# Optimization experiments

Hardware: AMD Instinct MI355X
Metric: run time of the kernel (lower is better)

## Reference

```python
import jax, jax.numpy as jnp
import numpy as np

T, B, C, N, H = 4, 8, 256, 2048, 16
D = C // H          # head dim = 16
SCALE = 0.25        # fixed scale in SCA_AV
EPS = 1e-5          # BatchNorm eps


def _conv_bn(h_in, w, gamma, beta):
    """1x1 Conv1d (bias=False) + BatchNorm1d in training mode.
    h_in: [T,B,C,N]; w: [C_out,C_in]; BN stats over (T,B,N) per channel."""
    h = jnp.einsum('oc,tbcn->tbon', w, h_in)
    mean = h.mean(axis=(0, 1, 3), keepdims=True)
    var = ((h - mean) ** 2).mean(axis=(0, 1, 3), keepdims=True)
    return gamma[None, None, :, None] * (h - mean) * jax.lax.rsqrt(var + EPS) + beta[None, None, :, None]


def _spike(h, vth):
    # MyNode called once after reset: mem = 0/tau + h; spike = (mem >= vth)
    return (h >= vth).astype(h.dtype)


def _heads(z):
    # [T,B,C,N] -> [T,B,H,N,D] (channel index c = h*D + d, matching torch reshape)
    return z.reshape(T, B, H, D, N).transpose(0, 1, 2, 4, 3)


def setup_inputs() -> dict:
    key = jax.random.key(0)
    ks = jax.random.split(key, 16)
    s = 1.0 / np.sqrt(C)
    inp = {
        'x': jax.random.normal(ks[0], (T, B, C, N), jnp.float32),
        'y': jax.random.normal(ks[1], (T, B, C, N), jnp.float32),
        'q_w': jax.random.normal(ks[2], (C, C), jnp.float32) * s,
        'q_gamma': jnp.ones((C,), jnp.float32),
        'q_beta': jnp.zeros((C,), jnp.float32),
        'k_w': jax.random.normal(ks[3], (C, C), jnp.float32) * s,
        'k_gamma': jnp.ones((C,), jnp.float32),
        'k_beta': jnp.zeros((C,), jnp.float32),
        'v_w': jax.random.normal(ks[4], (C, C), jnp.float32) * s,
        'v_gamma': jnp.ones((C,), jnp.float32),
        'v_beta': jnp.zeros((C,), jnp.float32),
        'proj_w': jax.random.normal(ks[5], (C, C), jnp.float32) * s,
        'proj_gamma': jnp.ones((C,), jnp.float32),
        'proj_beta': jnp.zeros((C,), jnp.float32),
    }
    return inp


def reference(x, y, q_w, q_gamma, q_beta, k_w, k_gamma, k_beta,
              v_w, v_gamma, v_beta, proj_w, proj_gamma, proj_beta):
    # spiking Q from x, spiking K/V from y
    q = _heads(_spike(_conv_bn(x, q_w, q_gamma, q_beta), 1.0))  # [T,B,H,N,D] in {0,1}
    k = _heads(_spike(_conv_bn(y, k_w, k_gamma, k_beta), 1.0))
    v = _heads(_spike(_conv_bn(y, v_w, v_gamma, v_beta), 1.0))
    # linear-attention reordering: (q @ k^T) @ v == q @ (k^T @ v); kv is only DxD
    kv = jnp.einsum('tbhnd,tbhne->tbhde', k, v)          # [T,B,H,D,D]
    o = jnp.einsum('tbhnd,tbhde->tbhne', q, kv) * SCALE  # [T,B,H,N,D]
    # back to [T,B,C,N] (transpose(3,4) then reshape, as in torch)
    o = o.transpose(0, 1, 2, 4, 3).reshape(T, B, C, N)
    s = _spike(o, 0.5)                                   # attn_lif, v_threshold=0.5
    out = _spike(_conv_bn(s, proj_w, proj_gamma, proj_beta), 1.0)  # proj + proj_lif
    return out
```

## Files before the change

### kernel.cpp

```cpp
#include <hip/hip_runtime.h>
#include <stdint.h>
#include <math.h>

#define T_ 4
#define B_ 8
#define C_ 256
#define N_ 2048
#define TB_ 32
#define H_ 16
#define D_ 16
#define NTOT 65536
#define EPS 1e-5
#define NSLOT 1024

typedef int v4i __attribute__((ext_vector_type(4)));

__global__ __launch_bounds__(256) void wprep_kernel(const float* __restrict__ W0,
                                                    const float* __restrict__ W1,
                                                    const float* __restrict__ W2,
                                                    int8_t* __restrict__ out) {
  const float* Wm = (blockIdx.y == 0) ? W0 : ((blockIdx.y == 1) ? W1 : W2);
  const int o = blockIdx.x;
  const int c = (int)threadIdx.x;
  double rr = rint((double)Wm[o * C_ + c] * 0x1p40);
  int8_t* base = out + (size_t)blockIdx.y * 5 * C_ * C_;
#pragma unroll
  for (int L = 0; L < 5; ++L) {
    const double q = floor(fma(rr, 0.00390625, 0.5));
    const double d = fma(q, -256.0, rr);
    base[(size_t)L * C_ * C_ + o * C_ + c] = (int8_t)(int)d;
    rr = q;
  }
}

__global__ __launch_bounds__(256) void conv_i8_qkv(const int8_t* __restrict__ Wl,
                                                   const float* __restrict__ X,
                                                   double* __restrict__ Hout,
                                                   double* __restrict__ Psum,
                                                   double* __restrict__ Psq) {
  __shared__ float Xs[64][81];
  __shared__ int8_t Wlds[5][64][80];
  __shared__ double dsum[4][64];
  __shared__ double dsq[4][64];
  const int n0 = blockIdx.x * 64;
  const int o0 = blockIdx.y * 64;
  const int tb = blockIdx.z;
  const int tid = (int)threadIdx.x;
  const int wv = tid >> 6;
  const int lane = tid & 63;
  const int l15 = lane & 15;
  const int g = lane >> 4;
  const int nn = 16 * wv + l15;

  const int c_l = tid >> 2;
  const int nc = tid & 3;

  const float* Xp = X + ((size_t)(tb * C_ + c_l)) * N_ + n0 + nc * 16;
  const int ws_o = tid >> 2;
  const int ws_c = (tid & 3) * 16;

  v4i acc[4][5] = {};

  for (int slab = 0; slab < 4; ++slab) {
    const int c0 = slab * 64;
    __syncthreads();
#pragma unroll
    for (int r = 0; r < 4; ++r) {
      const float4 xv = *(const float4*)(Xp + (size_t)c0 * N_ + 4 * r);
      Xs[c_l][nc * 16 + 4 * r + 0] = xv.x;
      Xs[c_l][nc * 16 + 4 * r + 1] = xv.y;
      Xs[c_l][nc * 16 + 4 * r + 2] = xv.z;
      Xs[c_l][nc * 16 + 4 * r + 3] = xv.w;
    }
#pragma unroll
    for (int L = 0; L < 5; ++L) {
      const int4 wchunk =
          *(const int4*)(Wl + (size_t)L * C_ * C_ + (size_t)(o0 + ws_o) * C_ + c0 + ws_c);
      *(int4*)&Wlds[L][ws_o][ws_c] = wchunk;
    }
    __syncthreads();

    uint32_t pk[4][4] = {};
#pragma unroll
    for (int s = 0; s < 16; ++s) {
      const float f = Xs[16 * g + s][nn];
      union { double d; unsigned long long u; } cv;
      cv.d = fma((double)f, 0x1p28, 0x1.8p52);
      int v = (int)(uint32_t)(cv.u & 0xffffffffULL);
      const int d0 = (int)(int8_t)v;  v = (v - d0) >> 8;
      const int d1 = (int)(int8_t)v;  v = (v - d1) >> 8;
      const int d2 = (int)(int8_t)v;
      const int d3 = (v - d2) >> 8;
      const int sh = 8 * (s & 3);
      const int w = s >> 2;
      pk[0][w] |= (uint32_t)(d0 & 255) << sh;
      pk[1][w] |= (uint32_t)(d1 & 255) << sh;
      pk[2][w] |= (uint32_t)(d2 & 255) << sh;
      pk[3][w] |= (uint32_t)(d3 & 255) << sh;
    }
    v4i Bf[4];
#pragma unroll
    for (int j = 0; j < 4; ++j)
      Bf[j] = (v4i){(int)pk[j][0], (int)pk[j][1], (int)pk[j][2], (int)pk[j][3]};

#pragma unroll
    for (int mt = 0; mt < 4; ++mt) {
      v4i A[5];
#pragma unroll
      for (int i = 0; i < 5; ++i)
        A[i] = *(const v4i*)&Wlds[i][16 * mt + l15][16 * g];
#pragma unroll
      for (int i = 0; i < 5; ++i)
#pragma unroll
        for (int j = 0; j < 4; ++j)
          if (i + j >= 3)
            acc[mt][i + j - 3] =
                __builtin_amdgcn_mfma_i32_16x16x64_i8(A[i], Bf[j], acc[mt][i + j - 3], 0, 0, 0);
    }
  }

  const double scale[5] = {0x1p-44, 0x1p-36, 0x1p-28, 0x1p-20, 0x1p-12};
#pragma unroll
  for (int mt = 0; mt < 4; ++mt) {
    double s[4], q[4];
#pragma unroll
    for (int r = 0; r < 4; ++r) {
      double v = 0.0;
#pragma unroll
      for (int a = 0; a < 5; ++a) v = fma(scale[a], (double)acc[mt][a][r], v);
      const int row = o0 + 16 * mt + 4 * g + r;
      Hout[((size_t)(tb * C_ + row)) * N_ + n0 + nn] = v;
      s[r] = v;
      q[r] = v * v;
    }
#pragma unroll
    for (int m = 1; m < 16; m <<= 1) {
#pragma unroll
      for (int r = 0; r < 4; ++r) {
        s[r] += __shfl_xor(s[r], m);
        q[r] += __shfl_xor(q[r], m);
      }
    }
    if (l15 < 4) {
      const int r = l15;
      dsum[wv][16 * mt + 4 * g + r] = s[r];
      dsq[wv][16 * mt + 4 * g + r] = q[r];
    }
  }
  __syncthreads();
  if (tid < 64) {
    const double S = dsum[0][tid] + dsum[1][tid] + dsum[2][tid] + dsum[3][tid];
    const double Q = dsq[0][tid] + dsq[1][tid] + dsq[2][tid] + dsq[3][tid];
    const int slot = tb * 32 + (int)blockIdx.x;
    Psum[(size_t)(o0 + tid) * NSLOT + slot] = S;
    Psq[(size_t)(o0 + tid) * NSLOT + slot] = Q;
  }
}

__global__ __launch_bounds__(256) void conv_i8_proj(const int8_t* __restrict__ Wl,
                                                    const uint8_t* __restrict__ S,
                                                    double* __restrict__ Hout,
                                                    double* __restrict__ Psum,
                                                    double* __restrict__ Psq) {
  __shared__ int8_t X1s[64][80];
  const int n0 = blockIdx.x * 64;
  const int o0 = blockIdx.y * 64;
  const int tb = blockIdx.z;
  const int tid = (int)threadIdx.x;
  const int wv = tid >> 6;
  const int lane = tid & 63;
  const int l15 = lane & 15;
  const int g = lane >> 4;

  const int c_l = tid >> 2;
  const int nc = tid & 3;

  v4i acc[4][5] = {};

  for (int slab = 0; slab < 4; ++slab) {
    const int c0 = slab * 64;
    v4i A[5];
#pragma unroll
    for (int i = 0; i < 5; ++i)
      A[i] = *(const v4i*)(Wl + ((size_t)i * C_ + o0 + 16 * wv + l15) * C_ + c0 + 16 * g);

    __syncthreads();
    {
      const int4 sv = *(const int4*)(S + ((size_t)(tb * C_ + c0 + c_l)) * N_ + n0 + nc * 16);
      const int8_t* sb = (const int8_t*)&sv;
#pragma unroll
      for (int j = 0; j < 16; ++j) X1s[nc * 16 + j][c_l] = sb[j];
    }
    __syncthreads();

#pragma unroll
    for (int t = 0; t < 4; ++t) {
      const v4i Bf = *(const v4i*)&X1s[16 * t + l15][16 * g];
#pragma unroll
      for (int i = 0; i < 5; ++i)
        acc[t][i] = __builtin_amdgcn_mfma_i32_16x16x64_i8(A[i], Bf, acc[t][i], 0, 0, 0);
    }
  }

  const double scale[5] = {0x1p-40, 0x1p-32, 0x1p-24, 0x1p-16, 0x1p-8};
  double s[4] = {0.0, 0.0, 0.0, 0.0};
  double q[4] = {0.0, 0.0, 0.0, 0.0};
#pragma unroll
  for (int t = 0; t < 4; ++t) {
#pragma unroll
    for (int r = 0; r < 4; ++r) {
      double v = 0.0;
#pragma unroll
      for (int a = 0; a < 5; ++a) v = fma(scale[a], (double)acc[t][a][r], v);
      const int row = o0 + 16 * wv + 4 * g + r;
      Hout[((size_t)(tb * C_ + row)) * N_ + n0 + 16 * t + l15] = v;
      s[r] += v;
      q[r] += v * v;
    }
  }
#pragma unroll
  for (int m = 1; m < 16; m <<= 1) {
#pragma unroll
    for (int r = 0; r < 4; ++r) {
      s[r] += __shfl_xor(s[r], m);
      q[r] += __shfl_xor(q[r], m);
    }
  }
  if (l15 < 4) {
    const int r = l15;
    const int c = o0 + 16 * wv + 4 * g + r;
    const int slot = tb * 32 + (int)blockIdx.x;
    Psum[(size_t)c * NSLOT + slot] = s[r];
    Psq[(size_t)c * NSLOT + slot] = q[r];
  }
}

__global__ __launch_bounds__(256) void finalize_stats(const double* __restrict__ Psum,
                                                      const double* __restrict__ Psq,
                                                      double* __restrict__ mean,
                                                      double* __restrict__ invstd) {
  const int c = blockIdx.x;
  const int tid = (int)threadIdx.x;
  double s = 0.0, q = 0.0;
  for (int i = tid; i < NSLOT; i += 256) {
    s += Psum[(size_t)c * NSLOT + i];
    q += Psq[(size_t)c * NSLOT + i];
  }
#pragma unroll
  for (int m = 1; m < 64; m <<= 1) {
    s += __shfl_xor(s, m);
    q += __shfl_xor(q, m);
  }
  __shared__ double ls[4], lq[4];
  if ((tid & 63) == 0) {
    ls[tid >> 6] = s;
    lq[tid >> 6] = q;
  }
  __syncthreads();
  if (tid == 0) {
    const double S = ls[0] + ls[1] + ls[2] + ls[3];
    const double Q = lq[0] + lq[1] + lq[2] + lq[3];
    const double m = S / (double)NTOT;
    const double var = Q / (double)NTOT - m * m;
    mean[c] = m;
    invstd[c] = 1.0 / sqrt(var + EPS);
  }
}

template <typename OT>
__device__ inline void store8(OT* p, const int* sp);
template <>
__device__ inline void store8<uint8_t>(uint8_t* p, const int* sp) {
  uint64_t w = 0;
#pragma unroll
  for (int j = 0; j < 8; ++j) w |= ((uint64_t)(uint8_t)sp[j]) << (8 * j);
  *(uint64_t*)p = w;
}
template <>
__device__ inline void store8<float>(float* p, const int* sp) {
  float4 a = make_float4((float)sp[0], (float)sp[1], (float)sp[2], (float)sp[3]);
  float4 b = make_float4((float)sp[4], (float)sp[5], (float)sp[6], (float)sp[7]);
  *(float4*)p = a;
  *(float4*)(p + 4) = b;
}

template <typename OT>
__global__ __launch_bounds__(256) void spike_kernel(const double* __restrict__ Hh,
                                                    const float* __restrict__ gamma,
                                                    const float* __restrict__ beta,
                                                    const double* __restrict__ mean,
                                                    const double* __restrict__ invstd,
                                                    OT* __restrict__ out) {
  const size_t i0 = ((size_t)blockIdx.x * 256 + threadIdx.x) * 8;
  const int c = (int)((i0 >> 11) & 255);
  const double gm = (double)gamma[c];
  const double bt = (double)beta[c];
  const double mu = mean[c];
  const double is = invstd[c];
  int sp[8];
#pragma unroll
  for (int j = 0; j < 8; ++j) {
    const double v = gm * (Hh[i0 + j] - mu) * is + bt;
    sp[j] = (v >= 1.0) ? 1 : 0;
  }
  store8<OT>(out + i0, sp);
}

__global__ __launch_bounds__(256) void attn_kernel(const uint8_t* __restrict__ Sq,
                                                   const uint8_t* __restrict__ Sk,
                                                   const uint8_t* __restrict__ Sv,
                                                   uint8_t* __restrict__ Sout) {
  __shared__ float kvs[16][17];
  const int tb = (int)blockIdx.x >> 4;
  const int h = (int)blockIdx.x & 15;
  const size_t base = ((size_t)(tb * C_ + h * D_)) * N_;
  const int tid = (int)threadIdx.x;
  {
    const int d = tid >> 4, e = tid & 15;
    const uint32_t* kr = (const uint32_t*)(Sk + base + (size_t)d * N_);
    const uint32_t* vr = (const uint32_t*)(Sv + base + (size_t)e * N_);
    int cnt = 0;
    for (int i = 0; i < N_ / 4; ++i) cnt += __popc(kr[i] & vr[i]);
    kvs[d][e] = (float)cnt;
  }
  __syncthreads();
  for (int rep = 0; rep < 8; ++rep) {
    const int n = rep * 256 + tid;
    float qv[16];
#pragma unroll
    for (int d = 0; d < 16; ++d) qv[d] = (float)Sq[base + (size_t)d * N_ + n];
#pragma unroll
    for (int e = 0; e < 16; ++e) {
      float acc = 0.f;
#pragma unroll
      for (int d = 0; d < 16; ++d) acc += qv[d] * kvs[d][e];
      Sout[base + (size_t)e * N_ + n] = (0.25f * acc >= 0.5f) ? (uint8_t)1 : (uint8_t)0;
    }
  }
}

extern "C" void kernel_launch(void* const* d_in, const int* in_sizes, int n_in,
                              void* d_out, int out_size, void* d_ws, size_t ws_size,
                              hipStream_t stream) {
  const float* x   = (const float*)d_in[0];
  const float* y   = (const float*)d_in[1];
  const float* q_w = (const float*)d_in[2];
  const float* q_g = (const float*)d_in[3];
  const float* q_b = (const float*)d_in[4];
  const float* k_w = (const float*)d_in[5];
  const float* k_g = (const float*)d_in[6];
  const float* k_b = (const float*)d_in[7];
  const float* v_w = (const float*)d_in[8];
  const float* v_g = (const float*)d_in[9];
  const float* v_b = (const float*)d_in[10];
  const float* p_w = (const float*)d_in[11];
  const float* p_g = (const float*)d_in[12];
  const float* p_b = (const float*)d_in[13];
  float* out = (float*)d_out;

  char* ws = (char*)d_ws;
  const size_t NE = (size_t)TB_ * C_ * N_;
  double* h64   = (double*)ws;
  uint8_t* Sq   = (uint8_t*)(ws + NE * 8);
  uint8_t* Sk   = Sq + NE;
  uint8_t* Sv   = Sk + NE;
  uint8_t* Sbuf = Sv + NE;

  double* PsumA   = (double*)Sbuf;
  double* PsqA    = PsumA + (size_t)C_ * NSLOT;
  double* meanA   = PsqA + (size_t)C_ * NSLOT;
  double* invstdA = meanA + C_;
  int8_t* WlA     = (int8_t*)(Sbuf + 8 * 1024 * 1024);
  int8_t* Wl_q    = WlA;
  int8_t* Wl_k    = WlA + (size_t)5 * C_ * C_;
  int8_t* Wl_v    = WlA + (size_t)10 * C_ * C_;
  double* PsumB   = (double*)Sq;
  double* PsqB    = PsumB + (size_t)C_ * NSLOT;
  double* meanB   = PsqB + (size_t)C_ * NSLOT;
  double* invstdB = meanB + C_;
  int8_t* WlB     = (int8_t*)(Sq + 8 * 1024 * 1024);

  const dim3 gridG(N_ / 64, C_ / 64, TB_);
  const dim3 blk(256);
  const int spikeBlocks = (int)(NE / (256 * 8));

  wprep_kernel<<<dim3(C_, 3), blk, 0, stream>>>(q_w, k_w, v_w, WlA);
  conv_i8_qkv<<<gridG, blk, 0, stream>>>(Wl_q, x, h64, PsumA, PsqA);
  finalize_stats<<<C_, blk, 0, stream>>>(PsumA, PsqA, meanA, invstdA);
  spike_kernel<uint8_t><<<spikeBlocks, blk, 0, stream>>>(h64, q_g, q_b, meanA, invstdA, Sq);
  conv_i8_qkv<<<gridG, blk, 0, stream>>>(Wl_k, y, h64, PsumA, PsqA);
  finalize_stats<<<C_, blk, 0, stream>>>(PsumA, PsqA, meanA, invstdA);
  spike_kernel<uint8_t><<<spikeBlocks, blk, 0, stream>>>(h64, k_g, k_b, meanA, invstdA, Sk);
  conv_i8_qkv<<<gridG, blk, 0, stream>>>(Wl_v, y, h64, PsumA, PsqA);
  finalize_stats<<<C_, blk, 0, stream>>>(PsumA, PsqA, meanA, invstdA);
  spike_kernel<uint8_t><<<spikeBlocks, blk, 0, stream>>>(h64, v_g, v_b, meanA, invstdA, Sv);
  attn_kernel<<<TB_ * H_, blk, 0, stream>>>(Sq, Sk, Sv, Sbuf);
  wprep_kernel<<<dim3(C_, 1), blk, 0, stream>>>(p_w, p_w, p_w, WlB);
  conv_i8_proj<<<gridG, blk, 0, stream>>>(WlB, Sbuf, h64, PsumB, PsqB);
  finalize_stats<<<C_, blk, 0, stream>>>(PsumB, PsqB, meanB, invstdB);
  spike_kernel<float><<<spikeBlocks, blk, 0, stream>>>(h64, p_g, p_b, meanB, invstdB, out);
}
```

Before: 810.0 us.

## Recompute int8 convolutions instead of materializing fp64 pre-BN activations

```diff
diff --git a/kernel.cpp b/kernel.cpp
--- a/kernel.cpp
+++ b/kernel.cpp
@@ -12,6 +12,7 @@
 #define NTOT 65536
 #define EPS 1e-5
 #define NSLOT 1024
+#define WPSZ 327680
 
 typedef int v4i __attribute__((ext_vector_type(4)));
 
@@ -23,67 +24,43 @@
   const int o = blockIdx.x;
   const int c = (int)threadIdx.x;
   double rr = rint((double)Wm[o * C_ + c] * 0x1p40);
-  int8_t* base = out + (size_t)blockIdx.y * 5 * C_ * C_;
+  int8_t* base = out + (size_t)blockIdx.y * WPSZ + (size_t)(c >> 4) * 20480 +
+                 (size_t)o * 80 + (c & 15);
 #pragma unroll
   for (int L = 0; L < 5; ++L) {
     const double q = floor(fma(rr, 0.00390625, 0.5));
     const double d = fma(q, -256.0, rr);
-    base[(size_t)L * C_ * C_ + o * C_ + c] = (int8_t)(int)d;
+    base[L * 16] = (int8_t)(int)d;
     rr = q;
   }
 }
 
-__global__ __launch_bounds__(256) void conv_i8_qkv(const int8_t* __restrict__ Wl,
-                                                   const float* __restrict__ X,
-                                                   double* __restrict__ Hout,
-                                                   double* __restrict__ Psum,
-                                                   double* __restrict__ Psq) {
+__global__ __launch_bounds__(256) void xprep_kernel(const float* __restrict__ X,
+                                                    uint8_t* __restrict__ XP) {
   __shared__ float Xs[64][81];
-  __shared__ int8_t Wlds[5][64][80];
-  __shared__ double dsum[4][64];
-  __shared__ double dsq[4][64];
   const int n0 = blockIdx.x * 64;
-  const int o0 = blockIdx.y * 64;
-  const int tb = blockIdx.z;
+  const int tb = blockIdx.y;
   const int tid = (int)threadIdx.x;
-  const int wv = tid >> 6;
-  const int lane = tid & 63;
-  const int l15 = lane & 15;
-  const int g = lane >> 4;
-  const int nn = 16 * wv + l15;
-
-  const int c_l = tid >> 2;
-  const int nc = tid & 3;
+  const int c_l = tid >> 2, nc = tid & 3;
+  const int n_l = tid & 63, cq = tid >> 6;
 
   const float* Xp = X + ((size_t)(tb * C_ + c_l)) * N_ + n0 + nc * 16;
-  const int ws_o = tid >> 2;
-  const int ws_c = (tid & 3) * 16;
-
-  v4i acc[4][5] = {};
 
   for (int slab = 0; slab < 4; ++slab) {
-    const int c0 = slab * 64;
     __syncthreads();
 #pragma unroll
     for (int r = 0; r < 4; ++r) {
-      const float4 xv = *(const float4*)(Xp + (size_t)c0 * N_ + 4 * r);
+      const float4 xv = *(const float4*)(Xp + (size_t)(slab * 64) * N_ + 4 * r);
       Xs[c_l][nc * 16 + 4 * r + 0] = xv.x;
       Xs[c_l][nc * 16 + 4 * r + 1] = xv.y;
       Xs[c_l][nc * 16 + 4 * r + 2] = xv.z;
       Xs[c_l][nc * 16 + 4 * r + 3] = xv.w;
     }
-#pragma unroll
-    for (int L = 0; L < 5; ++L) {
-      const int4 wchunk =
-          *(const int4*)(Wl + (size_t)L * C_ * C_ + (size_t)(o0 + ws_o) * C_ + c0 + ws_c);
-      *(int4*)&Wlds[L][ws_o][ws_c] = wchunk;
-    }
     __syncthreads();
-
     uint32_t pk[4][4] = {};
 #pragma unroll
     for (int s = 0; s < 16; ++s) {
-      const float f = Xs[16 * g + s][nn];
+      const float f = Xs[cq * 16 + s][n_l];
       union { double d; unsigned long long u; } cv;
       cv.d = fma((double)f, 0x1p28, 0x1.8p52);
       int v = (int)(uint32_t)(cv.u & 0xffffffffULL);
@@ -98,71 +75,27 @@
       pk[2][w] |= (uint32_t)(d2 & 255) << sh;
       pk[3][w] |= (uint32_t)(d3 & 255) << sh;
     }
-    v4i Bf[4];
-#pragma unroll
-    for (int j = 0; j < 4; ++j)
-      Bf[j] = (v4i){(int)pk[j][0], (int)pk[j][1], (int)pk[j][2], (int)pk[j][3]};
-
-#pragma unroll
-    for (int mt = 0; mt < 4; ++mt) {
-      v4i A[5];
-#pragma unroll
-      for (int i = 0; i < 5; ++i)
-        A[i] = *(const v4i*)&Wlds[i][16 * mt + l15][16 * g];
-#pragma unroll
-      for (int i = 0; i < 5; ++i)
-#pragma unroll
-        for (int j = 0; j < 4; ++j)
-          if (i + j >= 3)
-            acc[mt][i + j - 3] =
-                __builtin_amdgcn_mfma_i32_16x16x64_i8(A[i], Bf[j], acc[mt][i + j - 3], 0, 0, 0);
-    }
-  }
-
-  const double scale[5] = {0x1p-44, 0x1p-36, 0x1p-28, 0x1p-20, 0x1p-12};
-#pragma unroll
-  for (int mt = 0; mt < 4; ++mt) {
-    double s[4], q[4];
-#pragma unroll
-    for (int r = 0; r < 4; ++r) {
-      double v = 0.0;
-#pragma unroll
-      for (int a = 0; a < 5; ++a) v = fma(scale[a], (double)acc[mt][a][r], v);
-      const int row = o0 + 16 * mt + 4 * g + r;
-      Hout[((size_t)(tb * C_ + row)) * N_ + n0 + nn] = v;
-      s[r] = v;
-      q[r] = v * v;
-    }
-#pragma unroll
-    for (int m = 1; m < 16; m <<= 1) {
-#pragma unroll
-      for (int r = 0; r < 4; ++r) {
-        s[r] += __shfl_xor(s[r], m);
-        q[r] += __shfl_xor(q[r], m);
-      }
-    }
-    if (l15 < 4) {
-      const int r = l15;
-      dsum[wv][16 * mt + 4 * g + r] = s[r];
-      dsq[wv][16 * mt + 4 * g + r] = q[r];
-    }
-  }
-  __syncthreads();
-  if (tid < 64) {
-    const double S = dsum[0][tid] + dsum[1][tid] + dsum[2][tid] + dsum[3][tid];
-    const double Q = dsq[0][tid] + dsq[1][tid] + dsq[2][tid] + dsq[3][tid];
-    const int slot = tb * 32 + (int)blockIdx.x;
-    Psum[(size_t)(o0 + tid) * NSLOT + slot] = S;
-    Psq[(size_t)(o0 + tid) * NSLOT + slot] = Q;
-  }
-}
-
-__global__ __launch_bounds__(256) void conv_i8_proj(const int8_t* __restrict__ Wl,
-                                                    const uint8_t* __restrict__ S,
-                                                    double* __restrict__ Hout,
-                                                    double* __restrict__ Psum,
-                                                    double* __restrict__ Psq) {
-  __shared__ int8_t X1s[64][80];
+    uint8_t* dst =
+        XP + (((size_t)(tb * 16 + slab * 4 + cq)) * (size_t)N_ + n0 + n_l) * 64;
+#pragma unroll
+    for (int j = 0; j < 4; ++j) {
+      const int4 wv = make_int4((int)pk[j][0], (int)pk[j][1], (int)pk[j][2], (int)pk[j][3]);
+      *(int4*)(dst + 16 * j) = wv;
+    }
+  }
+}
+
+template <bool QKV, bool STATS, typename OutT>
+__global__ __launch_bounds__(256) void conv_i8(
+    const int8_t* __restrict__ WP, const uint8_t* __restrict__ BP,
+    double* __restrict__ Psum, double* __restrict__ Psq,
+    const float* __restrict__ gamma, const float* __restrict__ beta,
+    const double* __restrict__ mean, const double* __restrict__ invstd,
+    OutT* __restrict__ Out) {
+  __shared__ double dsum[4][64];
+  __shared__ double dsq[4][64];
+  __shared__ double aS[64];
+  __shared__ double bS[64];
   const int n0 = blockIdx.x * 64;
   const int o0 = blockIdx.y * 64;
   const int tb = blockIdx.z;
@@ -171,67 +104,102 @@
   const int lane = tid & 63;
   const int l15 = lane & 15;
   const int g = lane >> 4;
-
-  const int c_l = tid >> 2;
-  const int nc = tid & 3;
+  const int nn = 16 * wv + l15;
+
+  if constexpr (!STATS) {
+    if (tid < 64) {
+      const int c = o0 + tid;
+      const double is = invstd[c], mu = mean[c];
+      const double gm = (double)gamma[c], bt = (double)beta[c];
+      aS[tid] = gm * is;
+      bS[tid] = bt - gm * mu * is;
+    }
+    __syncthreads();
+  }
 
   v4i acc[4][5] = {};
 
   for (int slab = 0; slab < 4; ++slab) {
-    const int c0 = slab * 64;
-    v4i A[5];
-#pragma unroll
-    for (int i = 0; i < 5; ++i)
-      A[i] = *(const v4i*)(Wl + ((size_t)i * C_ + o0 + 16 * wv + l15) * C_ + c0 + 16 * g);
-
+    const int cc = slab * 4 + g;
+    v4i Bf[4];
+    if constexpr (QKV) {
+      const uint8_t* bp = BP + (((size_t)(tb * 16 + cc)) * (size_t)N_ + n0 + nn) * 64;
+#pragma unroll
+      for (int j = 0; j < 4; ++j) Bf[j] = *(const v4i*)(bp + 16 * j);
+    } else {
+      Bf[0] = *(const v4i*)(BP + ((size_t)(tb * N_ + n0 + nn)) * 256 + slab * 64 + 16 * g);
+    }
+#pragma unroll
+    for (int mt = 0; mt < 4; ++mt) {
+      const int8_t* ap = WP + (size_t)cc * 20480 + (size_t)(o0 + 16 * mt + l15) * 80;
+      v4i A[5];
+#pragma unroll
+      for (int i = 0; i < 5; ++i) A[i] = *(const v4i*)(ap + 16 * i);
+      if constexpr (QKV) {
+        constexpr int PI[14] = {0, 1, 2, 3, 4, 1, 2, 3, 4, 2, 3, 4, 3, 4};
+        constexpr int PJ[14] = {3, 3, 3, 3, 3, 2, 2, 2, 2, 1, 1, 1, 0, 0};
+#pragma unroll
+        for (int p = 0; p < 14; ++p)
+          acc[mt][PI[p] + PJ[p] - 3] = __builtin_amdgcn_mfma_i32_16x16x64_i8(
+              A[PI[p]], Bf[PJ[p]], acc[mt][PI[p] + PJ[p] - 3], 0, 0, 0);
+      } else {
+#pragma unroll
+        for (int i = 0; i < 5; ++i)
+          acc[mt][i] = __builtin_amdgcn_mfma_i32_16x16x64_i8(A[i], Bf[0], acc[mt][i], 0, 0, 0);
+      }
+    }
+  }
+
+  const double scale[5] = {QKV ? 0x1p-44 : 0x1p-40, QKV ? 0x1p-36 : 0x1p-32,
+                           QKV ? 0x1p-28 : 0x1p-24, QKV ? 0x1p-20 : 0x1p-16,
+                           QKV ? 0x1p-12 : 0x1p-8};
+
+  if constexpr (STATS) {
+#pragma unroll
+    for (int mt = 0; mt < 4; ++mt) {
+      double s[4], q[4];
+#pragma unroll
+      for (int r = 0; r < 4; ++r) {
+        double v = 0.0;
+#pragma unroll
+        for (int a = 0; a < 5; ++a) v = fma(scale[a], (double)acc[mt][a][r], v);
+        s[r] = v;
+        q[r] = v * v;
+      }
+#pragma unroll
+      for (int m = 1; m < 16; m <<= 1) {
+#pragma unroll
+        for (int r = 0; r < 4; ++r) {
+          s[r] += __shfl_xor(s[r], m);
+          q[r] += __shfl_xor(q[r], m);
+        }
+      }
+      if (l15 < 4) {
+        dsum[wv][16 * mt + 4 * g + l15] = s[l15];
+        dsq[wv][16 * mt + 4 * g + l15] = q[l15];
+      }
+    }
     __syncthreads();
-    {
-      const int4 sv = *(const int4*)(S + ((size_t)(tb * C_ + c0 + c_l)) * N_ + n0 + nc * 16);
-      const int8_t* sb = (const int8_t*)&sv;
-#pragma unroll
-      for (int j = 0; j < 16; ++j) X1s[nc * 16 + j][c_l] = sb[j];
-    }
-    __syncthreads();
-
-#pragma unroll
-    for (int t = 0; t < 4; ++t) {
-      const v4i Bf = *(const v4i*)&X1s[16 * t + l15][16 * g];
-#pragma unroll
-      for (int i = 0; i < 5; ++i)
-        acc[t][i] = __builtin_amdgcn_mfma_i32_16x16x64_i8(A[i], Bf, acc[t][i], 0, 0, 0);
-    }
-  }
-
-  const double scale[5] = {0x1p-40, 0x1p-32, 0x1p-24, 0x1p-16, 0x1p-8};
-  double s[4] = {0.0, 0.0, 0.0, 0.0};
-  double q[4] = {0.0, 0.0, 0.0, 0.0};
-#pragma unroll
-  for (int t = 0; t < 4; ++t) {
-#pragma unroll
-    for (int r = 0; r < 4; ++r) {
-      double v = 0.0;
-#pragma unroll
-      for (int a = 0; a < 5; ++a) v = fma(scale[a], (double)acc[t][a][r], v);
-      const int row = o0 + 16 * wv + 4 * g + r;
-      Hout[((size_t)(tb * C_ + row)) * N_ + n0 + 16 * t + l15] = v;
-      s[r] += v;
-      q[r] += v * v;
-    }
-  }
-#pragma unroll
-  for (int m = 1; m < 16; m <<= 1) {
-#pragma unroll
-    for (int r = 0; r < 4; ++r) {
-      s[r] += __shfl_xor(s[r], m);
-      q[r] += __shfl_xor(q[r], m);
-    }
-  }
-  if (l15 < 4) {
-    const int r = l15;
-    const int c = o0 + 16 * wv + 4 * g + r;
-    const int slot = tb * 32 + (int)blockIdx.x;
-    Psum[(size_t)c * NSLOT + slot] = s[r];
-    Psq[(size_t)c * NSLOT + slot] = q[r];
+    if (tid < 64) {
+      const double S = dsum[0][tid] + dsum[1][tid] + dsum[2][tid] + dsum[3][tid];
+      const double Q = dsq[0][tid] + dsq[1][tid] + dsq[2][tid] + dsq[3][tid];
+      const int slot = tb * 32 + (int)blockIdx.x;
+      Psum[(size_t)(o0 + tid) * NSLOT + slot] = S;
+      Psq[(size_t)(o0 + tid) * NSLOT + slot] = Q;
+    }
+  } else {
+#pragma unroll
+    for (int mt = 0; mt < 4; ++mt) {
+#pragma unroll
+      for (int r = 0; r < 4; ++r) {
+        double v = 0.0;
+#pragma unroll
+        for (int a = 0; a < 5; ++a) v = fma(scale[a], (double)acc[mt][a][r], v);
+        const int row = 16 * mt + 4 * g + r;
+        const int sp = (aS[row] * v + bS[row] >= 1.0) ? 1 : 0;
+        Out[((size_t)(tb * C_ + o0 + row)) * N_ + n0 + nn] = (OutT)sp;
+      }
+    }
   }
 }
 
@@ -267,49 +235,10 @@
   }
 }
 
-template <typename OT>
-__device__ inline void store8(OT* p, const int* sp);
-template <>
-__device__ inline void store8<uint8_t>(uint8_t* p, const int* sp) {
-  uint64_t w = 0;
-#pragma unroll
-  for (int j = 0; j < 8; ++j) w |= ((uint64_t)(uint8_t)sp[j]) << (8 * j);
-  *(uint64_t*)p = w;
-}
-template <>
-__device__ inline void store8<float>(float* p, const int* sp) {
-  float4 a = make_float4((float)sp[0], (float)sp[1], (float)sp[2], (float)sp[3]);
-  float4 b = make_float4((float)sp[4], (float)sp[5], (float)sp[6], (float)sp[7]);
-  *(float4*)p = a;
-  *(float4*)(p + 4) = b;
-}
-
-template <typename OT>
-__global__ __launch_bounds__(256) void spike_kernel(const double* __restrict__ Hh,
-                                                    const float* __restrict__ gamma,
-                                                    const float* __restrict__ beta,
-                                                    const double* __restrict__ mean,
-                                                    const double* __restrict__ invstd,
-                                                    OT* __restrict__ out) {
-  const size_t i0 = ((size_t)blockIdx.x * 256 + threadIdx.x) * 8;
-  const int c = (int)((i0 >> 11) & 255);
-  const double gm = (double)gamma[c];
-  const double bt = (double)beta[c];
-  const double mu = mean[c];
-  const double is = invstd[c];
-  int sp[8];
-#pragma unroll
-  for (int j = 0; j < 8; ++j) {
-    const double v = gm * (Hh[i0 + j] - mu) * is + bt;
-    sp[j] = (v >= 1.0) ? 1 : 0;
-  }
-  store8<OT>(out + i0, sp);
-}
-
 __global__ __launch_bounds__(256) void attn_kernel(const uint8_t* __restrict__ Sq,
                                                    const uint8_t* __restrict__ Sk,
                                                    const uint8_t* __restrict__ Sv,
-                                                   uint8_t* __restrict__ Sout) {
+                                                   uint8_t* __restrict__ SbufT) {
   __shared__ float kvs[16][17];
   const int tb = (int)blockIdx.x >> 4;
   const int h = (int)blockIdx.x & 15;
@@ -329,13 +258,17 @@
     float qv[16];
 #pragma unroll
     for (int d = 0; d < 16; ++d) qv[d] = (float)Sq[base + (size_t)d * N_ + n];
+    uint32_t w[4] = {0, 0, 0, 0};
 #pragma unroll
     for (int e = 0; e < 16; ++e) {
       float acc = 0.f;
 #pragma unroll
       for (int d = 0; d < 16; ++d) acc += qv[d] * kvs[d][e];
-      Sout[base + (size_t)e * N_ + n] = (0.25f * acc >= 0.5f) ? (uint8_t)1 : (uint8_t)0;
-    }
+      const uint32_t sp = (0.25f * acc >= 0.5f) ? 1u : 0u;
+      w[e >> 2] |= sp << (8 * (e & 3));
+    }
+    const int4 pw = make_int4((int)w[0], (int)w[1], (int)w[2], (int)w[3]);
+    *(int4*)(SbufT + ((size_t)(tb * N_ + n)) * 256 + h * 16) = pw;
   }
 }
 
@@ -360,43 +293,53 @@
 
   char* ws = (char*)d_ws;
   const size_t NE = (size_t)TB_ * C_ * N_;
-  double* h64   = (double*)ws;
-  uint8_t* Sq   = (uint8_t*)(ws + NE * 8);
-  uint8_t* Sk   = Sq + NE;
-  uint8_t* Sv   = Sk + NE;
-  uint8_t* Sbuf = Sv + NE;
-
-  double* PsumA   = (double*)Sbuf;
+  uint8_t* XPx   = (uint8_t*)ws;
+  uint8_t* XPy   = (uint8_t*)(ws + NE * 4);
+  uint8_t* Sq    = (uint8_t*)(ws + NE * 8);
+  uint8_t* Sk    = Sq + NE;
+  uint8_t* Sv    = Sk + NE;
+  uint8_t* SbufT = Sv + NE;
+
+  double* PsumA   = (double*)SbufT;
   double* PsqA    = PsumA + (size_t)C_ * NSLOT;
   double* meanA   = PsqA + (size_t)C_ * NSLOT;
   double* invstdA = meanA + C_;
-  int8_t* WlA     = (int8_t*)(Sbuf + 8 * 1024 * 1024);
-  int8_t* Wl_q    = WlA;
-  int8_t* Wl_k    = WlA + (size_t)5 * C_ * C_;
-  int8_t* Wl_v    = WlA + (size_t)10 * C_ * C_;
+  int8_t* WPA     = (int8_t*)(SbufT + 5 * 1024 * 1024);
+  int8_t* WPq     = WPA;
+  int8_t* WPk     = WPA + WPSZ;
+  int8_t* WPv     = WPA + 2 * WPSZ;
   double* PsumB   = (double*)Sq;
   double* PsqB    = PsumB + (size_t)C_ * NSLOT;
   double* meanB   = PsqB + (size_t)C_ * NSLOT;
   double* invstdB = meanB + C_;
-  int8_t* WlB     = (int8_t*)(Sq + 8 * 1024 * 1024);
+  int8_t* WPB     = (int8_t*)(Sq + 8 * 1024 * 1024);
 
   const dim3 gridG(N_ / 64, C_ / 64, TB_);
   const dim3 blk(256);
-  const int spikeBlocks = (int)(NE / (256 * 8));
-
-  wprep_kernel<<<dim3(C_, 3), blk, 0, stream>>>(q_w, k_w, v_w, WlA);
-  conv_i8_qkv<<<gridG, blk, 0, stream>>>(Wl_q, x, h64, PsumA, PsqA);
+
+  wprep_kernel<<<dim3(C_, 3), blk, 0, stream>>>(q_w, k_w, v_w, WPA);
+  xprep_kernel<<<dim3(N_ / 64, TB_), blk, 0, stream>>>(x, XPx);
+  xprep_kernel<<<dim3(N_ / 64, TB_), blk, 0, stream>>>(y, XPy);
+  conv_i8<true, true, uint8_t><<<gridG, blk, 0, stream>>>(
+      WPq, XPx, PsumA, PsqA, nullptr, nullptr, nullptr, nullptr, (uint8_t*)nullptr);
   finalize_stats<<<C_, blk, 0, stream>>>(PsumA, PsqA, meanA, invstdA);
-  spike_kernel<uint8_t><<<spikeBlocks, blk, 0, stream>>>(h64, q_g, q_b, meanA, invstdA, Sq);
-  conv_i8_qkv<<<gridG, blk, 0, stream>>>(Wl_k, y, h64, PsumA, PsqA);
+  conv_i8<true, false, uint8_t><<<gridG, blk, 0, stream>>>(
+      WPq, XPx, nullptr, nullptr, q_g, q_b, meanA, invstdA, Sq);
+  conv_i8<true, true, uint8_t><<<gridG, blk, 0, stream>>>(
+      WPk, XPy, PsumA, PsqA, nullptr, nullptr, nullptr, nullptr, (uint8_t*)nullptr);
   finalize_stats<<<C_, blk, 0, stream>>>(PsumA, PsqA, meanA, invstdA);
-  spike_kernel<uint8_t><<<spikeBlocks, blk, 0, stream>>>(h64, k_g, k_b, meanA, invstdA, Sk);
-  conv_i8_qkv<<<gridG, blk, 0, stream>>>(Wl_v, y, h64, PsumA, PsqA);
+  conv_i8<true, false, uint8_t><<<gridG, blk, 0, stream>>>(
+      WPk, XPy, nullptr, nullptr, k_g, k_b, meanA, invstdA, Sk);
+  conv_i8<true, true, uint8_t><<<gridG, blk, 0, stream>>>(
+      WPv, XPy, PsumA, PsqA, nullptr, nullptr, nullptr, nullptr, (uint8_t*)nullptr);
   finalize_stats<<<C_, blk, 0, stream>>>(PsumA, PsqA, meanA, invstdA);
-  spike_kernel<uint8_t><<<spikeBlocks, blk, 0, stream>>>(h64, v_g, v_b, meanA, invstdA, Sv);
-  attn_kernel<<<TB_ * H_, blk, 0, stream>>>(Sq, Sk, Sv, Sbuf);
-  wprep_kernel<<<dim3(C_, 1), blk, 0, stream>>>(p_w, p_w, p_w, WlB);
-  conv_i8_proj<<<gridG, blk, 0, stream>>>(WlB, Sbuf, h64, PsumB, PsqB);
+  conv_i8<true, false, uint8_t><<<gridG, blk, 0, stream>>>(
+      WPv, XPy, nullptr, nullptr, v_g, v_b, meanA, invstdA, Sv);
+  attn_kernel<<<TB_ * H_, blk, 0, stream>>>(Sq, Sk, Sv, SbufT);
+  wprep_kernel<<<dim3(C_, 1), blk, 0, stream>>>(p_w, p_w, p_w, WPB);
+  conv_i8<false, true, float><<<gridG, blk, 0, stream>>>(
+      WPB, SbufT, PsumB, PsqB, nullptr, nullptr, nullptr, nullptr, (float*)nullptr);
   finalize_stats<<<C_, blk, 0, stream>>>(PsumB, PsqB, meanB, invstdB);
-  spike_kernel<float><<<spikeBlocks, blk, 0, stream>>>(h64, p_g, p_b, meanB, invstdB, out);
-}
+  conv_i8<false, false, float><<<gridG, blk, 0, stream>>>(
+      WPB, SbufT, nullptr, nullptr, p_g, p_b, meanB, invstdB, out);
+}
```

After: 821.9 us. No clear change (+1.5%).
